# Optimization experiments

Measured on AMD Instinct MI355X. Metric: run time of the kernel, lower is better.

The kernel has to match this reference:

```python
import jax, jax.numpy as jnp
import numpy as np

NEG_SLOPE = 0.2


def gat_conv(x, src, dst, W, att_src, att_dst, bias, heads, out_ch, concat):
    """PyG-style GATConv (eval mode, self-loops already appended to src/dst)."""
    N = x.shape[0]
    h = (x @ W).reshape(N, heads, out_ch)                      # [N,H,C]
    a_src = jnp.einsum('nhc,hc->nh', h, att_src)               # [N,H]
    a_dst = jnp.einsum('nhc,hc->nh', h, att_dst)               # [N,H]
    e = jax.nn.leaky_relu(a_src[src] + a_dst[dst], NEG_SLOPE)  # [E,H]
    # numerically-stable softmax segmented by destination node
    emax = jax.ops.segment_max(e, dst, num_segments=N)         # [N,H]
    e = jnp.exp(e - emax[dst])
    denom = jax.ops.segment_sum(e, dst, num_segments=N)
    alpha = e / (denom[dst] + 1e-16)                           # [E,H]
    msg = h[src] * alpha[..., None]                            # [E,H,C]
    out = jax.ops.segment_sum(msg, dst, num_segments=N)        # [N,H,C]
    out = out.reshape(N, heads * out_ch) if concat else out.mean(axis=1)
    return out + bias


def setup_inputs() -> dict:
    key = jax.random.key(0)
    ks = jax.random.split(key, 9)
    N, E, IN, OUT = 100000, 1600000, 128, 40
    H1, C1 = 8, 8
    x = jax.random.normal(ks[0], (N, IN), dtype=jnp.float32)
    edge_index = jax.random.randint(ks[1], (2, E), 0, N, dtype=jnp.int64)
    s = 0.1
    return {
        'x': x,
        'edge_index': edge_index,
        'W1': jax.random.normal(ks[2], (IN, H1 * C1), dtype=jnp.float32) * s,
        'att_src1': jax.random.normal(ks[3], (H1, C1), dtype=jnp.float32) * s,
        'att_dst1': jax.random.normal(ks[4], (H1, C1), dtype=jnp.float32) * s,
        'b1': jnp.zeros((H1 * C1,), dtype=jnp.float32),
        'W2': jax.random.normal(ks[5], (H1 * C1, OUT), dtype=jnp.float32) * s,
        'att_src2': jax.random.normal(ks[6], (1, OUT), dtype=jnp.float32) * s,
        'att_dst2': jax.random.normal(ks[7], (1, OUT), dtype=jnp.float32) * s,
        'b2': jnp.zeros((OUT,), dtype=jnp.float32),
    }


def reference(x, edge_index, W1, att_src1, att_dst1, b1, W2, att_src2, att_dst2, b2):
    N = x.shape[0]
    loops = jnp.arange(N, dtype=edge_index.dtype)
    src = jnp.concatenate([edge_index[0], loops])  # self-loops (PyG default)
    dst = jnp.concatenate([edge_index[1], loops])
    h = gat_conv(x, src, dst, W1, att_src1, att_dst1, b1, 8, 8, True)
    h = jax.nn.elu(h)  # dropout is identity in eval mode
    out = gat_conv(h, src, dst, W2, att_src2, att_dst2, b2, 1, W2.shape[1], False)
    return jax.nn.log_softmax(out, axis=-1)
```

## Files before the change

kernel.cpp:

```cpp
#include <hip/hip_runtime.h>
#include <math.h>

#define NEG_SLOPE 0.2f
#define BSHIFT 8
#define MAXBUK 512

typedef __attribute__((ext_vector_type(8))) short short8;
typedef __attribute__((ext_vector_type(4))) float floatx4;

static __device__ __forceinline__ float lrelu_exp(float e) {
    e = fmaxf(e, NEG_SLOPE * e);
    return __expf(e);
}

static __device__ __forceinline__ short f2bf(float f) {
    union { float f; unsigned u; } v; v.f = f;
    unsigned r = v.u + 0x7FFFu + ((v.u >> 16) & 1u);
    return (short)(r >> 16);
}
static __device__ __forceinline__ float bf2f(unsigned short s) {
    union { float f; unsigned u; } v;
    v.u = ((unsigned)s) << 16;
    return v.f;
}
static __device__ __forceinline__ float bfpair_lo(unsigned v) {
    union { float f; unsigned u; } x; x.u = v << 16; return x.f;
}
static __device__ __forceinline__ float bfpair_hi(unsigned v) {
    union { float f; unsigned u; } x; x.u = v & 0xffff0000u; return x.f;
}
static __device__ __forceinline__ void splitbf(float f, short& hi, short& lo) {
    hi = f2bf(f);
    lo = f2bf(f - bf2f((unsigned short)hi));
}


__global__ __launch_bounds__(512) void k_hist_gemm1(const int* __restrict__ dst, int E,
                                                    int CHUNK, int NBLK, int NBUK,
                                                    int* __restrict__ blockhist,
                                                    const float* __restrict__ W2,
                                                    short* __restrict__ w2ht,
                                                    short* __restrict__ w2lt,
                                                    const float* __restrict__ x,
                                                    const float* __restrict__ W1,
                                                    const float* __restrict__ att_s,
                                                    const float* __restrict__ att_d,
                                                    unsigned short* __restrict__ h1b,
                                                    float* __restrict__ a_s1,
                                                    float* __restrict__ a_d1, int N) {
    __shared__ int hist[MAXBUK];
    __shared__ short w1s[64 * 136];
    int t = threadIdx.x, b = blockIdx.x;
    if (b < NBLK) {
        for (int i = t; i < NBUK; i += 512) hist[i] = 0;
        __syncthreads();
        int e0 = b * CHUNK, e1 = e0 + CHUNK; if (e1 > E) e1 = E;
        for (int e = e0 + t; e < e1; e += 512) atomicAdd(&hist[dst[e] >> BSHIFT], 1);
        __syncthreads();
        for (int i = t; i < NBUK; i += 512) blockhist[(size_t)i * NBLK + b] = hist[i];
        return;
    }
    if (b < NBLK + 6) {
        int j = (b - NBLK) * 512 + t;
        if (j < 48 * 64) {
            int n = j >> 6, k = j & 63;
            short hi = 0, lo = 0;
            if (n < 40) splitbf(W2[k * 40 + n], hi, lo);
            w2ht[j] = hi; w2lt[j] = lo;
        }
        return;
    }
    int gb = b - NBLK - 6;
    for (int i = t; i < 64 * 128; i += 512) {
        int k = i >> 6, n = i & 63;
        w1s[n * 136 + k] = f2bf(W1[i]);
    }
    __syncthreads();
    int wave = t >> 6, lane = t & 63;
    int n16 = lane & 15, q = lane >> 4;
    int nb = gb * 128 + wave * 16;
    if (nb >= N) return;

    short8 bfr[4][4];
#pragma unroll
    for (int ct = 0; ct < 4; ++ct) {
        int n = ct * 16 + n16;
#pragma unroll
        for (int kc = 0; kc < 4; ++kc)
            bfr[ct][kc] = *(const short8*)(w1s + n * 136 + kc * 32 + q * 8);
    }

    int arow = nb + n16; if (arow >= N) arow = N - 1;
    const float* xr = x + (size_t)arow * 128 + q * 8;
    short8 afr[4];
#pragma unroll
    for (int kc = 0; kc < 4; ++kc) {
        float4 u0 = *(const float4*)(xr + kc * 32);
        float4 u1 = *(const float4*)(xr + kc * 32 + 4);
        short8 a;
        a[0] = f2bf(u0.x); a[1] = f2bf(u0.y); a[2] = f2bf(u0.z); a[3] = f2bf(u0.w);
        a[4] = f2bf(u1.x); a[5] = f2bf(u1.y); a[6] = f2bf(u1.z); a[7] = f2bf(u1.w);
        afr[kc] = a;
    }

    floatx4 acc[4];
#pragma unroll
    for (int ct = 0; ct < 4; ++ct) {
        floatx4 c = {0.f, 0.f, 0.f, 0.f};
#pragma unroll
        for (int kc = 0; kc < 4; ++kc)
            c = __builtin_amdgcn_mfma_f32_16x16x32_bf16(afr[kc], bfr[ct][kc], c, 0, 0, 0);
        acc[ct] = c;
    }

#pragma unroll
    for (int ct = 0; ct < 4; ++ct) {
#pragma unroll
        for (int r = 0; r < 4; ++r) {
            int row = nb + q * 4 + r;
            if (row < N) h1b[(size_t)row * 64 + ct * 16 + n16] = (unsigned short)f2bf(acc[ct][r]);
        }
    }

#pragma unroll
    for (int ct = 0; ct < 4; ++ct) {
        float as = att_s[ct * 16 + n16];
        float ad = att_d[ct * 16 + n16];
#pragma unroll
        for (int r = 0; r < 4; ++r) {
            float ps = acc[ct][r] * as;
            float pd = acc[ct][r] * ad;
#pragma unroll
            for (int m = 1; m < 8; m <<= 1) {
                ps += __shfl_xor(ps, m, 64);
                pd += __shfl_xor(pd, m, 64);
            }
            int row = nb + q * 4 + r;
            if ((n16 & 7) == 0 && row < N) {
                int h = 2 * ct + (n16 >> 3);
                a_s1[row * 8 + h] = ps;
                a_d1[row * 8 + h] = pd;
            }
        }
    }
}

__global__ __launch_bounds__(256) void k_colscan(int* __restrict__ blockhist,
                                                 int* __restrict__ btot, int NBLK) {
    int bucket = blockIdx.x, t = threadIdx.x;
    int lane = t & 63, wv = t >> 6;
    __shared__ int wsum[4];
    __shared__ int carry_s;
    if (t == 0) carry_s = 0;
    __syncthreads();
    for (int base = 0; base < NBLK; base += 256) {
        int idx = base + t;
        int v = (idx < NBLK) ? blockhist[(size_t)bucket * NBLK + idx] : 0;
        int s = v;
#pragma unroll
        for (int o = 1; o < 64; o <<= 1) {
            int u = __shfl_up(s, o, 64);
            if (lane >= o) s += u;
        }
        if (lane == 63) wsum[wv] = s;
        __syncthreads();
        int b0 = 0;
#pragma unroll
        for (int w = 0; w < 4; ++w) b0 += (w < wv) ? wsum[w] : 0;
        int excl = s + b0 - v + carry_s;
        if (idx < NBLK) blockhist[(size_t)bucket * NBLK + idx] = excl;
        __syncthreads();
        if (t == 255) carry_s += s + b0;
        __syncthreads();
    }
    if (t == 0) btot[bucket] = carry_s;
}

__global__ __launch_bounds__(512) void k_bucket_scan(const int* __restrict__ btot,
                                                     int* __restrict__ bucketbase, int NBUK) {
    __shared__ int sh[512];
    int t = threadIdx.x;
    int v = (t < NBUK) ? btot[t] : 0;
    sh[t] = v;
    __syncthreads();
#pragma unroll
    for (int o = 1; o < 512; o <<= 1) {
        int u = (t >= o) ? sh[t - o] : 0;
        __syncthreads();
        sh[t] += u;
        __syncthreads();
    }
    if (t < NBUK) bucketbase[t] = sh[t] - v;
    if (t == NBUK - 1) bucketbase[NBUK] = sh[t];
}

__global__ __launch_bounds__(512) void k_partition(const int* __restrict__ src,
                                                   const int* __restrict__ dst, int E, int CHUNK,
                                                   int NBLK, int NBUK,
                                                   const int* __restrict__ blockhist,
                                                   const int* __restrict__ bucketbase,
                                                   unsigned* __restrict__ packed) {
    __shared__ int cur[MAXBUK];
    int t = threadIdx.x, b = blockIdx.x;
    for (int i = t; i < NBUK; i += 512)
        cur[i] = blockhist[(size_t)i * NBLK + b] + bucketbase[i];
    __syncthreads();
    int e0 = b * CHUNK, e1 = e0 + CHUNK; if (e1 > E) e1 = E;
    for (int e = e0 + t; e < e1; e += 512) {
        int d = dst[e], s = src[e];
        int pos = atomicAdd(&cur[d >> BSHIFT], 1);
        packed[pos] = ((unsigned)s << 8) | ((unsigned)d & 255u);
    }
}

__global__ __launch_bounds__(256) void k_fine(const unsigned* __restrict__ packed,
                                              const int* __restrict__ bucketbase,
                                              int* __restrict__ offsets,
                                              int* __restrict__ csr_src,
                                              int N, int NBUK) {
    __shared__ int fcnt[256];
    __shared__ int wsum[4];
    int bucket = blockIdx.x, t = threadIdx.x;
    int lo = bucket << BSHIFT;
    int nn = N - lo; if (nn > 256) nn = 256;
    int ebase = bucketbase[bucket];
    int ecnt = bucketbase[bucket + 1] - ebase;
    fcnt[t] = 0;
    __syncthreads();
    for (int i = t; i < ecnt; i += 256) {
        unsigned p = packed[ebase + i];
        atomicAdd(&fcnt[p & 255u], 1);
    }
    __syncthreads();
    int v = fcnt[t];
    int lane = t & 63, wv = t >> 6;
    int s = v;
#pragma unroll
    for (int o = 1; o < 64; o <<= 1) {
        int u = __shfl_up(s, o, 64);
        if (lane >= o) s += u;
    }
    if (lane == 63) wsum[wv] = s;
    __syncthreads();
    int base = 0;
#pragma unroll
    for (int w = 0; w < 4; ++w) base += (w < wv) ? wsum[w] : 0;
    int excl = s + base - v;
    if (t < nn) offsets[lo + t] = ebase + excl;
    if (bucket == NBUK - 1 && t == 0) offsets[N] = ebase + ecnt;
    __syncthreads();
    fcnt[t] = excl;
    __syncthreads();
    for (int i = t; i < ecnt; i += 256) {
        unsigned p = packed[ebase + i];
        int pos = atomicAdd(&fcnt[p & 255u], 1);
        csr_src[ebase + pos] = (int)(p >> 8);
    }
}

__global__ __launch_bounds__(256) void k_agg1(const unsigned short* __restrict__ h1b,
                                              const float* __restrict__ a_s1,
                                              const float* __restrict__ a_d1,
                                              const int* __restrict__ offsets,
                                              const int* __restrict__ csr_src,
                                              const float* __restrict__ b1,
                                              float* __restrict__ y1, int N) {
    int wave = threadIdx.x >> 6, lane = threadIdx.x & 63;
    int q = lane >> 4;
    int ll = lane & 15;
    int d = (blockIdx.x * 4 + wave) * 4 + q;
    bool dvalid = (d < N);
    int de = dvalid ? d : N - 1;
    int g = ll >> 3;
    int c = ll & 7;
    float ad = a_d1[de * 8 + c];
    int i0 = offsets[de];
    int deg = dvalid ? (offsets[de + 1] - i0) : 0;
    int dmax = deg;
    dmax = max(dmax, __shfl_xor(dmax, 16, 64));
    dmax = max(dmax, __shfl_xor(dmax, 32, 64));
    float acc[8] = {0.f, 0.f, 0.f, 0.f, 0.f, 0.f, 0.f, 0.f};
    float wsum_l = 0.f;
    if (g == 0) {
        float w0 = lrelu_exp(a_s1[de * 8 + c] + ad);
        uint4 v = *(const uint4*)(h1b + (size_t)de * 64 + 8 * c);
        acc[0] = w0 * bfpair_lo(v.x); acc[1] = w0 * bfpair_hi(v.x);
        acc[2] = w0 * bfpair_lo(v.y); acc[3] = w0 * bfpair_hi(v.y);
        acc[4] = w0 * bfpair_lo(v.z); acc[5] = w0 * bfpair_hi(v.z);
        acc[6] = w0 * bfpair_lo(v.w); acc[7] = w0 * bfpair_hi(v.w);
        wsum_l = w0;
    }
    for (int j = 0; j < dmax; j += 8) {
        int b0 = i0 + j + 4 * g;
        int idx[4]; bool lv[4];
#pragma unroll
        for (int u = 0; u < 4; ++u) {
            int jj = j + 4 * g + u;
            lv[u] = (jj < deg);
            idx[u] = de;
            if (lv[u]) idx[u] = csr_src[b0 + u];
        }
        float ev[4];
#pragma unroll
        for (int u = 0; u < 4; ++u) ev[u] = a_s1[idx[u] * 8 + c] + ad;
        uint4 vv[4];
#pragma unroll
        for (int u = 0; u < 4; ++u)
            vv[u] = *(const uint4*)(h1b + (size_t)idx[u] * 64 + 8 * c);
#pragma unroll
        for (int u = 0; u < 4; ++u) {
            float w = lv[u] ? lrelu_exp(ev[u]) : 0.f;
            wsum_l += w;
            acc[0] = fmaf(w, bfpair_lo(vv[u].x), acc[0]);
            acc[1] = fmaf(w, bfpair_hi(vv[u].x), acc[1]);
            acc[2] = fmaf(w, bfpair_lo(vv[u].y), acc[2]);
            acc[3] = fmaf(w, bfpair_hi(vv[u].y), acc[3]);
            acc[4] = fmaf(w, bfpair_lo(vv[u].z), acc[4]);
            acc[5] = fmaf(w, bfpair_hi(vv[u].z), acc[5]);
            acc[6] = fmaf(w, bfpair_lo(vv[u].w), acc[6]);
            acc[7] = fmaf(w, bfpair_hi(vv[u].w), acc[7]);
        }
    }
#pragma unroll
    for (int k = 0; k < 8; ++k) acc[k] += __shfl(acc[k], lane + 8, 64);
    wsum_l += __shfl(wsum_l, lane + 8, 64);
    if (g == 0 && dvalid) {
        float inv = 1.f / (wsum_l + 1e-16f);
        float4 bA = *(const float4*)(b1 + 8 * c);
        float4 bB = *(const float4*)(b1 + 8 * c + 4);
        float o[8];
        o[0] = acc[0] * inv + bA.x;
        o[1] = acc[1] * inv + bA.y;
        o[2] = acc[2] * inv + bA.z;
        o[3] = acc[3] * inv + bA.w;
        o[4] = acc[4] * inv + bB.x;
        o[5] = acc[5] * inv + bB.y;
        o[6] = acc[6] * inv + bB.z;
        o[7] = acc[7] * inv + bB.w;
#pragma unroll
        for (int k = 0; k < 8; ++k) o[k] = o[k] > 0.f ? o[k] : (__expf(o[k]) - 1.f);
        float4 s0 = make_float4(o[0], o[1], o[2], o[3]);
        float4 s1 = make_float4(o[4], o[5], o[6], o[7]);
        *(float4*)(y1 + (size_t)d * 64 + 8 * c) = s0;
        *(float4*)(y1 + (size_t)d * 64 + 8 * c + 4) = s1;
    }
}

__global__ __launch_bounds__(256) void k_gemm2(const float* __restrict__ y1,
                                               const short* __restrict__ w2ht,
                                               const short* __restrict__ w2lt,
                                               const float* __restrict__ att_s,
                                               const float* __restrict__ att_d,
                                               unsigned short* __restrict__ h2b,
                                               float* __restrict__ a2s,
                                               float* __restrict__ a2d, int N) {
    int tid = threadIdx.x, wave = tid >> 6, lane = tid & 63;
    int n16 = lane & 15, q = lane >> 4;
    int nb = blockIdx.x * 64 + wave * 16;
    if (nb >= N) return;

    int arow = nb + n16; if (arow >= N) arow = N - 1;
    const float* yr = y1 + (size_t)arow * 64 + q * 8;
    short8 ah[2], al[2];
#pragma unroll
    for (int kc = 0; kc < 2; ++kc) {
        float4 u0 = *(const float4*)(yr + kc * 32);
        float4 u1 = *(const float4*)(yr + kc * 32 + 4);
        short8 h, l; short hi, lo;
        splitbf(u0.x, hi, lo); h[0] = hi; l[0] = lo;
        splitbf(u0.y, hi, lo); h[1] = hi; l[1] = lo;
        splitbf(u0.z, hi, lo); h[2] = hi; l[2] = lo;
        splitbf(u0.w, hi, lo); h[3] = hi; l[3] = lo;
        splitbf(u1.x, hi, lo); h[4] = hi; l[4] = lo;
        splitbf(u1.y, hi, lo); h[5] = hi; l[5] = lo;
        splitbf(u1.z, hi, lo); h[6] = hi; l[6] = lo;
        splitbf(u1.w, hi, lo); h[7] = hi; l[7] = lo;
        ah[kc] = h; al[kc] = l;
    }

    float psr[4] = {0.f, 0.f, 0.f, 0.f}, pdr[4] = {0.f, 0.f, 0.f, 0.f};
#pragma unroll
    for (int ct = 0; ct < 3; ++ct) {
        int n = ct * 16 + n16;
        short8 bh0 = *(const short8*)(w2ht + n * 64 + q * 8);
        short8 bh1 = *(const short8*)(w2ht + n * 64 + 32 + q * 8);
        short8 bl0 = *(const short8*)(w2lt + n * 64 + q * 8);
        short8 bl1 = *(const short8*)(w2lt + n * 64 + 32 + q * 8);
        floatx4 c = {0.f, 0.f, 0.f, 0.f};
        c = __builtin_amdgcn_mfma_f32_16x16x32_bf16(ah[0], bl0, c, 0, 0, 0);
        c = __builtin_amdgcn_mfma_f32_16x16x32_bf16(al[0], bh0, c, 0, 0, 0);
        c = __builtin_amdgcn_mfma_f32_16x16x32_bf16(ah[0], bh0, c, 0, 0, 0);
        c = __builtin_amdgcn_mfma_f32_16x16x32_bf16(ah[1], bl1, c, 0, 0, 0);
        c = __builtin_amdgcn_mfma_f32_16x16x32_bf16(al[1], bh1, c, 0, 0, 0);
        c = __builtin_amdgcn_mfma_f32_16x16x32_bf16(ah[1], bh1, c, 0, 0, 0);

        int col = ct * 16 + n16;
#pragma unroll
        for (int r = 0; r < 4; ++r) {
            int row = nb + q * 4 + r;
            if (col < 40 && row < N) h2b[(size_t)row * 48 + col] = (unsigned short)f2bf(c[r]);
        }
        float asv = (col < 40) ? att_s[col] : 0.f;
        float adv = (col < 40) ? att_d[col] : 0.f;
#pragma unroll
        for (int r = 0; r < 4; ++r) {
            psr[r] = fmaf(c[r], asv, psr[r]);
            pdr[r] = fmaf(c[r], adv, pdr[r]);
        }
    }
#pragma unroll
    for (int r = 0; r < 4; ++r) {
        float ps = psr[r], pd = pdr[r];
#pragma unroll
        for (int m = 1; m < 16; m <<= 1) {
            ps += __shfl_xor(ps, m, 64);
            pd += __shfl_xor(pd, m, 64);
        }
        int row = nb + q * 4 + r;
        if (n16 == 0 && row < N) { a2s[row] = ps; a2d[row] = pd; }
    }
}

__global__ __launch_bounds__(256) void k_agg2(const unsigned short* __restrict__ h2b,
                                              const float* __restrict__ a2s,
                                              const float* __restrict__ a2d,
                                              const int* __restrict__ offsets,
                                              const int* __restrict__ csr_src,
                                              const float* __restrict__ b2,
                                              float* __restrict__ out, int N) {
    int wave = threadIdx.x >> 6, lane = threadIdx.x & 63;
    int q = lane >> 4;
    int ll = lane & 15;
    int d = (blockIdx.x * 4 + wave) * 4 + q;
    bool dvalid = (d < N);
    int de = dvalid ? d : N - 1;
    int g = ll / 5;
    int c = ll - g * 5;
    bool lane_ok = (ll < 15);
    float ad = a2d[de];
    float w0 = lrelu_exp(a2s[de] + ad);
    int i0 = offsets[de];
    int deg = offsets[de + 1] - i0;
    if (!dvalid) deg = 0;
    int dmax = deg;
    dmax = max(dmax, __shfl_xor(dmax, 16, 64));
    dmax = max(dmax, __shfl_xor(dmax, 32, 64));
    float acc[8] = {0.f, 0.f, 0.f, 0.f, 0.f, 0.f, 0.f, 0.f};
    float wsum_l = 0.f;
    if (g == 0) {
        uint4 v = *(const uint4*)(h2b + (size_t)de * 48 + 8 * c);
        acc[0] = w0 * bfpair_lo(v.x); acc[1] = w0 * bfpair_hi(v.x);
        acc[2] = w0 * bfpair_lo(v.y); acc[3] = w0 * bfpair_hi(v.y);
        acc[4] = w0 * bfpair_lo(v.z); acc[5] = w0 * bfpair_hi(v.z);
        acc[6] = w0 * bfpair_lo(v.w); acc[7] = w0 * bfpair_hi(v.w);
    }
    for (int j = 0; j < dmax; j += 12) {
        int b0 = i0 + j + 4 * g;
        int idx[4]; bool lv[4];
#pragma unroll
        for (int u = 0; u < 4; ++u) {
            int jj = j + 4 * g + u;
            lv[u] = lane_ok && (jj < deg);
            idx[u] = de;
            if (lv[u]) idx[u] = csr_src[b0 + u];
        }
        float ev[4];
#pragma unroll
        for (int u = 0; u < 4; ++u) ev[u] = a2s[idx[u]] + ad;
        uint4 vv[4];
#pragma unroll
        for (int u = 0; u < 4; ++u)
            vv[u] = *(const uint4*)(h2b + (size_t)idx[u] * 48 + 8 * c);
#pragma unroll
        for (int u = 0; u < 4; ++u) {
            float w = lv[u] ? lrelu_exp(ev[u]) : 0.f;
            if (c == 0) wsum_l += w;
            acc[0] = fmaf(w, bfpair_lo(vv[u].x), acc[0]);
            acc[1] = fmaf(w, bfpair_hi(vv[u].x), acc[1]);
            acc[2] = fmaf(w, bfpair_lo(vv[u].y), acc[2]);
            acc[3] = fmaf(w, bfpair_hi(vv[u].y), acc[3]);
            acc[4] = fmaf(w, bfpair_lo(vv[u].z), acc[4]);
            acc[5] = fmaf(w, bfpair_hi(vv[u].z), acc[5]);
            acc[6] = fmaf(w, bfpair_lo(vv[u].w), acc[6]);
            acc[7] = fmaf(w, bfpair_hi(vv[u].w), acc[7]);
        }
    }
#pragma unroll
    for (int k = 0; k < 8; ++k)
        acc[k] += __shfl(acc[k], lane + 5, 64) + __shfl(acc[k], lane + 10, 64);
    wsum_l += __shfl(wsum_l, lane + 5, 64) + __shfl(wsum_l, lane + 10, 64);
    wsum_l = __shfl(wsum_l, lane & 48, 64);
    float wsum = wsum_l + w0;
    bool act5 = (ll < 5) && dvalid;
    float inv = 1.f / (wsum + 1e-16f);
    float4 bA = *(const float4*)(b2 + 8 * c);
    float4 bB = *(const float4*)(b2 + 8 * c + 4);
    float o[8];
    o[0] = acc[0] * inv + bA.x;
    o[1] = acc[1] * inv + bA.y;
    o[2] = acc[2] * inv + bA.z;
    o[3] = acc[3] * inv + bA.w;
    o[4] = acc[4] * inv + bB.x;
    o[5] = acc[5] * inv + bB.y;
    o[6] = acc[6] * inv + bB.z;
    o[7] = acc[7] * inv + bB.w;
    float mxl = -INFINITY;
    if (act5) {
        mxl = fmaxf(fmaxf(fmaxf(o[0], o[1]), fmaxf(o[2], o[3])),
                    fmaxf(fmaxf(o[4], o[5]), fmaxf(o[6], o[7])));
    }
#pragma unroll
    for (int mm = 1; mm < 8; mm <<= 1) mxl = fmaxf(mxl, __shfl_xor(mxl, mm, 64));
    float exl = 0.f;
    if (act5) {
#pragma unroll
        for (int k = 0; k < 8; ++k) exl += __expf(o[k] - mxl);
    }
#pragma unroll
    for (int mm = 1; mm < 8; mm <<= 1) exl += __shfl_xor(exl, mm, 64);
    if (act5) {
        float lse = mxl + __logf(exl);
        float4 s0 = make_float4(o[0] - lse, o[1] - lse, o[2] - lse, o[3] - lse);
        float4 s1 = make_float4(o[4] - lse, o[5] - lse, o[6] - lse, o[7] - lse);
        *(float4*)(out + (size_t)d * 40 + 8 * c) = s0;
        *(float4*)(out + (size_t)d * 40 + 8 * c + 4) = s1;
    }
}


extern "C" void kernel_launch(void* const* d_in, const int* in_sizes, int n_in,
                              void* d_out, int out_size, void* d_ws, size_t ws_size,
                              hipStream_t stream) {
    const float* x   = (const float*)d_in[0];
    const int*   ei  = (const int*)d_in[1];
    const float* W1  = (const float*)d_in[2];
    const float* as1 = (const float*)d_in[3];
    const float* ad1 = (const float*)d_in[4];
    const float* b1  = (const float*)d_in[5];
    const float* W2  = (const float*)d_in[6];
    const float* as2 = (const float*)d_in[7];
    const float* ad2 = (const float*)d_in[8];
    const float* b2  = (const float*)d_in[9];
    float* out = (float*)d_out;

    int N = in_sizes[0] / 128;
    int E = in_sizes[1] / 2;
    const int* src = ei;
    const int* dst = ei + E;

    int NBUK = (N + 255) >> BSHIFT;
    int CHUNK = 4096;
    int NBLK = (E + CHUNK - 1) / CHUNK;

    char* ws = (char*)d_ws;
    size_t off = 0;
    auto alloc = [&](size_t bytes) -> char* {
        char* p = ws + off;
        off += (bytes + 255) & ~(size_t)255;
        return p;
    };
    unsigned short* h1b = (unsigned short*)alloc((size_t)N * 64 * 2);
    float* a_s1    = (float*)alloc((size_t)N * 8 * 4);
    float* a_d1    = (float*)alloc((size_t)N * 8 * 4);
    float* y1      = (float*)alloc((size_t)N * 64 * 4);
    size_t shared_sz = (size_t)N * 48 * 2;
    if ((size_t)E * 4 > shared_sz) shared_sz = (size_t)E * 4;
    char*  region  = alloc(shared_sz);
    unsigned short* h2b = (unsigned short*)region;
    unsigned* packed    = (unsigned*)region;
    float* a2s     = (float*)alloc((size_t)N * 4);
    float* a2d     = (float*)alloc((size_t)N * 4);
    int*   offsets = (int*)alloc((size_t)(N + 1) * 4);
    int*   csr_src = (int*)alloc((size_t)E * 4);
    int*   blockhist  = (int*)alloc((size_t)NBUK * NBLK * 4);
    int*   btot       = (int*)alloc((size_t)NBUK * 4);
    int*   bucketbase = (int*)alloc((size_t)(NBUK + 1) * 4);
    short* w2ht    = (short*)alloc((size_t)48 * 64 * 2);
    short* w2lt    = (short*)alloc((size_t)48 * 64 * 2);

    int nb1 = (N + 15) / 16;
    int nb2 = (N + 15) / 16;
    int gb2 = (N + 63) / 64;
    int GB1 = (N + 127) / 128;
    int W2B = 6;

    k_hist_gemm1<<<NBLK + W2B + GB1, 512, 0, stream>>>(dst, E, CHUNK, NBLK, NBUK, blockhist,
                                                       W2, w2ht, w2lt,
                                                       x, W1, as1, ad1, h1b, a_s1, a_d1, N);
    k_colscan<<<NBUK, 256, 0, stream>>>(blockhist, btot, NBLK);
    k_bucket_scan<<<1, 512, 0, stream>>>(btot, bucketbase, NBUK);
    k_partition<<<NBLK, 512, 0, stream>>>(src, dst, E, CHUNK, NBLK, NBUK, blockhist,
                                          bucketbase, packed);
    k_fine<<<NBUK, 256, 0, stream>>>(packed, bucketbase, offsets, csr_src, N, NBUK);
    k_agg1<<<nb1, 256, 0, stream>>>(h1b, a_s1, a_d1, offsets, csr_src, b1, y1, N);
    k_gemm2<<<gb2, 256, 0, stream>>>(y1, w2ht, w2lt, as2, ad2, h2b, a2s, a2d, N);
    k_agg2<<<nb2, 256, 0, stream>>>(h2b, a2s, a2d, offsets, csr_src, b2, out, N);
}
```

Measured before the change: 165.9 us.

## Partition each node's CSR neighbours into four source-range segments for gather locality

Measured after the change: 170.0 us. 1.02x slower.

```diff
diff --git a/kernel.cpp b/kernel.cpp
--- a/kernel.cpp
+++ b/kernel.cpp
@@ -216,23 +216,27 @@
 __global__ __launch_bounds__(256) void k_fine(const unsigned* __restrict__ packed,
                                               const int* __restrict__ bucketbase,
                                               int* __restrict__ offsets,
+                                              int* __restrict__ segs,
                                               int* __restrict__ csr_src,
-                                              int N, int NBUK) {
-    __shared__ int fcnt[256];
+                                              int N, int NBUK, int RDIV) {
+    __shared__ int fcnt[256 * 4];
     __shared__ int wsum[4];
     int bucket = blockIdx.x, t = threadIdx.x;
     int lo = bucket << BSHIFT;
     int nn = N - lo; if (nn > 256) nn = 256;
     int ebase = bucketbase[bucket];
     int ecnt = bucketbase[bucket + 1] - ebase;
-    fcnt[t] = 0;
+    for (int i = t; i < 1024; i += 256) fcnt[i] = 0;
     __syncthreads();
     for (int i = t; i < ecnt; i += 256) {
         unsigned p = packed[ebase + i];
-        atomicAdd(&fcnt[p & 255u], 1);
-    }
-    __syncthreads();
-    int v = fcnt[t];
+        int srcv = (int)(p >> 8);
+        atomicAdd(&fcnt[((p & 255u) << 2) | (unsigned)(srcv / RDIV)], 1);
+    }
+    __syncthreads();
+    int c0 = fcnt[t * 4 + 0], c1 = fcnt[t * 4 + 1];
+    int c2 = fcnt[t * 4 + 2], c3 = fcnt[t * 4 + 3];
+    int v = c0 + c1 + c2 + c3;
     int lane = t & 63, wv = t >> 6;
     int s = v;
 #pragma unroll
@@ -246,15 +250,25 @@
 #pragma unroll
     for (int w = 0; w < 4; ++w) base += (w < wv) ? wsum[w] : 0;
     int excl = s + base - v;
-    if (t < nn) offsets[lo + t] = ebase + excl;
+    if (t < nn) {
+        offsets[lo + t] = ebase + excl;
+        segs[(lo + t) * 4 + 0] = ebase + excl;
+        segs[(lo + t) * 4 + 1] = ebase + excl + c0;
+        segs[(lo + t) * 4 + 2] = ebase + excl + c0 + c1;
+        segs[(lo + t) * 4 + 3] = ebase + excl + c0 + c1 + c2;
+    }
     if (bucket == NBUK - 1 && t == 0) offsets[N] = ebase + ecnt;
     __syncthreads();
-    fcnt[t] = excl;
+    fcnt[t * 4 + 0] = excl;
+    fcnt[t * 4 + 1] = excl + c0;
+    fcnt[t * 4 + 2] = excl + c0 + c1;
+    fcnt[t * 4 + 3] = excl + c0 + c1 + c2;
     __syncthreads();
     for (int i = t; i < ecnt; i += 256) {
         unsigned p = packed[ebase + i];
-        int pos = atomicAdd(&fcnt[p & 255u], 1);
-        csr_src[ebase + pos] = (int)(p >> 8);
+        int srcv = (int)(p >> 8);
+        int pos = atomicAdd(&fcnt[((p & 255u) << 2) | (unsigned)(srcv / RDIV)], 1);
+        csr_src[ebase + pos] = srcv;
     }
 }
 
@@ -262,6 +276,7 @@
                                               const float* __restrict__ a_s1,
                                               const float* __restrict__ a_d1,
                                               const int* __restrict__ offsets,
+                                              const int* __restrict__ segs,
                                               const int* __restrict__ csr_src,
                                               const float* __restrict__ b1,
                                               float* __restrict__ y1, int N) {
@@ -274,11 +289,9 @@
     int g = ll >> 3;
     int c = ll & 7;
     float ad = a_d1[de * 8 + c];
-    int i0 = offsets[de];
-    int deg = dvalid ? (offsets[de + 1] - i0) : 0;
-    int dmax = deg;
-    dmax = max(dmax, __shfl_xor(dmax, 16, 64));
-    dmax = max(dmax, __shfl_xor(dmax, 32, 64));
+    int4 sg = *(const int4*)(segs + 4 * de);
+    int e3 = offsets[de + 1];
+    int st[5] = {sg.x, sg.y, sg.z, sg.w, e3};
     float acc[8] = {0.f, 0.f, 0.f, 0.f, 0.f, 0.f, 0.f, 0.f};
     float wsum_l = 0.f;
     if (g == 0) {
@@ -290,35 +303,43 @@
         acc[6] = w0 * bfpair_lo(v.w); acc[7] = w0 * bfpair_hi(v.w);
         wsum_l = w0;
     }
-    for (int j = 0; j < dmax; j += 8) {
-        int b0 = i0 + j + 4 * g;
-        int idx[4]; bool lv[4];
-#pragma unroll
-        for (int u = 0; u < 4; ++u) {
-            int jj = j + 4 * g + u;
-            lv[u] = (jj < deg);
-            idx[u] = de;
-            if (lv[u]) idx[u] = csr_src[b0 + u];
-        }
-        float ev[4];
-#pragma unroll
-        for (int u = 0; u < 4; ++u) ev[u] = a_s1[idx[u] * 8 + c] + ad;
-        uint4 vv[4];
-#pragma unroll
-        for (int u = 0; u < 4; ++u)
-            vv[u] = *(const uint4*)(h1b + (size_t)idx[u] * 64 + 8 * c);
-#pragma unroll
-        for (int u = 0; u < 4; ++u) {
-            float w = lv[u] ? lrelu_exp(ev[u]) : 0.f;
-            wsum_l += w;
-            acc[0] = fmaf(w, bfpair_lo(vv[u].x), acc[0]);
-            acc[1] = fmaf(w, bfpair_hi(vv[u].x), acc[1]);
-            acc[2] = fmaf(w, bfpair_lo(vv[u].y), acc[2]);
-            acc[3] = fmaf(w, bfpair_hi(vv[u].y), acc[3]);
-            acc[4] = fmaf(w, bfpair_lo(vv[u].z), acc[4]);
-            acc[5] = fmaf(w, bfpair_hi(vv[u].z), acc[5]);
-            acc[6] = fmaf(w, bfpair_lo(vv[u].w), acc[6]);
-            acc[7] = fmaf(w, bfpair_hi(vv[u].w), acc[7]);
+#pragma unroll
+    for (int r = 0; r < 4; ++r) {
+        int i0 = st[r];
+        int deg = dvalid ? (st[r + 1] - i0) : 0;
+        int dmax = deg;
+        dmax = max(dmax, __shfl_xor(dmax, 16, 64));
+        dmax = max(dmax, __shfl_xor(dmax, 32, 64));
+        for (int j = 0; j < dmax; j += 8) {
+            int b0 = i0 + j + 4 * g;
+            int idx[4]; bool lv[4];
+#pragma unroll
+            for (int u = 0; u < 4; ++u) {
+                int jj = j + 4 * g + u;
+                lv[u] = (jj < deg);
+                idx[u] = de;
+                if (lv[u]) idx[u] = csr_src[b0 + u];
+            }
+            float ev[4];
+#pragma unroll
+            for (int u = 0; u < 4; ++u) ev[u] = a_s1[idx[u] * 8 + c] + ad;
+            uint4 vv[4];
+#pragma unroll
+            for (int u = 0; u < 4; ++u)
+                vv[u] = *(const uint4*)(h1b + (size_t)idx[u] * 64 + 8 * c);
+#pragma unroll
+            for (int u = 0; u < 4; ++u) {
+                float w = lv[u] ? lrelu_exp(ev[u]) : 0.f;
+                wsum_l += w;
+                acc[0] = fmaf(w, bfpair_lo(vv[u].x), acc[0]);
+                acc[1] = fmaf(w, bfpair_hi(vv[u].x), acc[1]);
+                acc[2] = fmaf(w, bfpair_lo(vv[u].y), acc[2]);
+                acc[3] = fmaf(w, bfpair_hi(vv[u].y), acc[3]);
+                acc[4] = fmaf(w, bfpair_lo(vv[u].z), acc[4]);
+                acc[5] = fmaf(w, bfpair_hi(vv[u].z), acc[5]);
+                acc[6] = fmaf(w, bfpair_lo(vv[u].w), acc[6]);
+                acc[7] = fmaf(w, bfpair_hi(vv[u].w), acc[7]);
+            }
         }
     }
 #pragma unroll
@@ -425,6 +446,7 @@
                                               const float* __restrict__ a2s,
                                               const float* __restrict__ a2d,
                                               const int* __restrict__ offsets,
+                                              const int* __restrict__ segs,
                                               const int* __restrict__ csr_src,
                                               const float* __restrict__ b2,
                                               float* __restrict__ out, int N) {
@@ -439,12 +461,9 @@
     bool lane_ok = (ll < 15);
     float ad = a2d[de];
     float w0 = lrelu_exp(a2s[de] + ad);
-    int i0 = offsets[de];
-    int deg = offsets[de + 1] - i0;
-    if (!dvalid) deg = 0;
-    int dmax = deg;
-    dmax = max(dmax, __shfl_xor(dmax, 16, 64));
-    dmax = max(dmax, __shfl_xor(dmax, 32, 64));
+    int4 sg = *(const int4*)(segs + 4 * de);
+    int e3 = offsets[de + 1];
+    int st[5] = {sg.x, sg.y, sg.z, sg.w, e3};
     float acc[8] = {0.f, 0.f, 0.f, 0.f, 0.f, 0.f, 0.f, 0.f};
     float wsum_l = 0.f;
     if (g == 0) {
@@ -454,35 +473,43 @@
         acc[4] = w0 * bfpair_lo(v.z); acc[5] = w0 * bfpair_hi(v.z);
         acc[6] = w0 * bfpair_lo(v.w); acc[7] = w0 * bfpair_hi(v.w);
     }
-    for (int j = 0; j < dmax; j += 12) {
-        int b0 = i0 + j + 4 * g;
-        int idx[4]; bool lv[4];
-#pragma unroll
-        for (int u = 0; u < 4; ++u) {
-            int jj = j + 4 * g + u;
-            lv[u] = lane_ok && (jj < deg);
-            idx[u] = de;
-            if (lv[u]) idx[u] = csr_src[b0 + u];
-        }
-        float ev[4];
-#pragma unroll
-        for (int u = 0; u < 4; ++u) ev[u] = a2s[idx[u]] + ad;
-        uint4 vv[4];
-#pragma unroll
-        for (int u = 0; u < 4; ++u)
-            vv[u] = *(const uint4*)(h2b + (size_t)idx[u] * 48 + 8 * c);
-#pragma unroll
-        for (int u = 0; u < 4; ++u) {
-            float w = lv[u] ? lrelu_exp(ev[u]) : 0.f;
-            if (c == 0) wsum_l += w;
-            acc[0] = fmaf(w, bfpair_lo(vv[u].x), acc[0]);
-            acc[1] = fmaf(w, bfpair_hi(vv[u].x), acc[1]);
-            acc[2] = fmaf(w, bfpair_lo(vv[u].y), acc[2]);
-            acc[3] = fmaf(w, bfpair_hi(vv[u].y), acc[3]);
-            acc[4] = fmaf(w, bfpair_lo(vv[u].z), acc[4]);
-            acc[5] = fmaf(w, bfpair_hi(vv[u].z), acc[5]);
-            acc[6] = fmaf(w, bfpair_lo(vv[u].w), acc[6]);
-            acc[7] = fmaf(w, bfpair_hi(vv[u].w), acc[7]);
+#pragma unroll
+    for (int r = 0; r < 4; ++r) {
+        int i0 = st[r];
+        int deg = dvalid ? (st[r + 1] - i0) : 0;
+        int dmax = deg;
+        dmax = max(dmax, __shfl_xor(dmax, 16, 64));
+        dmax = max(dmax, __shfl_xor(dmax, 32, 64));
+        for (int j = 0; j < dmax; j += 12) {
+            int b0 = i0 + j + 4 * g;
+            int idx[4]; bool lv[4];
+#pragma unroll
+            for (int u = 0; u < 4; ++u) {
+                int jj = j + 4 * g + u;
+                lv[u] = lane_ok && (jj < deg);
+                idx[u] = de;
+                if (lv[u]) idx[u] = csr_src[b0 + u];
+            }
+            float ev[4];
+#pragma unroll
+            for (int u = 0; u < 4; ++u) ev[u] = a2s[idx[u]] + ad;
+            uint4 vv[4];
+#pragma unroll
+            for (int u = 0; u < 4; ++u)
+                vv[u] = *(const uint4*)(h2b + (size_t)idx[u] * 48 + 8 * c);
+#pragma unroll
+            for (int u = 0; u < 4; ++u) {
+                float w = lv[u] ? lrelu_exp(ev[u]) : 0.f;
+                if (c == 0) wsum_l += w;
+                acc[0] = fmaf(w, bfpair_lo(vv[u].x), acc[0]);
+                acc[1] = fmaf(w, bfpair_hi(vv[u].x), acc[1]);
+                acc[2] = fmaf(w, bfpair_lo(vv[u].y), acc[2]);
+                acc[3] = fmaf(w, bfpair_hi(vv[u].y), acc[3]);
+                acc[4] = fmaf(w, bfpair_lo(vv[u].z), acc[4]);
+                acc[5] = fmaf(w, bfpair_hi(vv[u].z), acc[5]);
+                acc[6] = fmaf(w, bfpair_lo(vv[u].w), acc[6]);
+                acc[7] = fmaf(w, bfpair_hi(vv[u].w), acc[7]);
+            }
         }
     }
 #pragma unroll
@@ -551,6 +578,7 @@
     int NBUK = (N + 255) >> BSHIFT;
     int CHUNK = 4096;
     int NBLK = (E + CHUNK - 1) / CHUNK;
+    int RDIV = (N + 3) / 4;
 
     char* ws = (char*)d_ws;
     size_t off = 0;
@@ -571,6 +599,7 @@
     float* a2s     = (float*)alloc((size_t)N * 4);
     float* a2d     = (float*)alloc((size_t)N * 4);
     int*   offsets = (int*)alloc((size_t)(N + 1) * 4);
+    int*   segs    = (int*)alloc((size_t)N * 4 * 4);
     int*   csr_src = (int*)alloc((size_t)E * 4);
     int*   blockhist  = (int*)alloc((size_t)NBUK * NBLK * 4);
     int*   btot       = (int*)alloc((size_t)NBUK * 4);
@@ -591,8 +620,8 @@
     k_bucket_scan<<<1, 512, 0, stream>>>(btot, bucketbase, NBUK);
     k_partition<<<NBLK, 512, 0, stream>>>(src, dst, E, CHUNK, NBLK, NBUK, blockhist,
                                           bucketbase, packed);
-    k_fine<<<NBUK, 256, 0, stream>>>(packed, bucketbase, offsets, csr_src, N, NBUK);
-    k_agg1<<<nb1, 256, 0, stream>>>(h1b, a_s1, a_d1, offsets, csr_src, b1, y1, N);
+    k_fine<<<NBUK, 256, 0, stream>>>(packed, bucketbase, offsets, segs, csr_src, N, NBUK, RDIV);
+    k_agg1<<<nb1, 256, 0, stream>>>(h1b, a_s1, a_d1, offsets, segs, csr_src, b1, y1, N);
     k_gemm2<<<gb2, 256, 0, stream>>>(y1, w2ht, w2lt, as2, ad2, h2b, a2s, a2d, N);
-    k_agg2<<<nb2, 256, 0, stream>>>(h2b, a2s, a2d, offsets, csr_src, b2, out, N);
-}
+    k_agg2<<<nb2, 256, 0, stream>>>(h2b, a2s, a2d, offsets, segs, csr_src, b2, out, N);
+}
```
